# Kernel optimization log

Measured on AMD Instinct MI355X. Metric: run time of the kernel, lower is better.

The kernel has to match this reference:

```python
import jax, jax.numpy as jnp
import numpy as np

D_MODEL = 1024
NUM_HEADS = 16


def setup_inputs() -> dict:
    key = jax.random.key(0)
    ks = jax.random.split(key, 5)
    B, N, D = 2, 2048, D_MODEL
    x = jax.random.normal(ks[0], (B, N, D), dtype=jnp.float32)
    Wq = jax.random.normal(ks[1], (D, D), dtype=jnp.float32) * 0.02
    Wk = jax.random.normal(ks[2], (D, D), dtype=jnp.float32) * 0.02
    Wv = jax.random.normal(ks[3], (D, D), dtype=jnp.float32) * 0.02
    Wo = jax.random.normal(ks[4], (D, D), dtype=jnp.float32) * 0.02
    return {"x": x, "Wq": Wq, "Wk": Wk, "Wv": Wv, "Wo": Wo}


def reference(x, Wq, Wk, Wv, Wo):
    # Executed path of QuantizedHyperbolicAttention.forward: TRITON_AVAILABLE is
    # False in the source, so the module always runs _pytorch_attention
    # (standard scaled-dot-product attention), mask=None.
    B, N, D = x.shape
    H = NUM_HEADS
    hd = D // H
    # nn.Linear(bias=False): y = x @ W.T
    q = (x @ Wq.T).reshape(B, N, H, hd).transpose(0, 2, 1, 3)  # [B,H,N,hd]
    k = (x @ Wk.T).reshape(B, N, H, hd).transpose(0, 2, 1, 3)
    v = (x @ Wv.T).reshape(B, N, H, hd).transpose(0, 2, 1, 3)
    scale = hd ** -0.5
    attn = jnp.einsum("bhnd,bhmd->bhnm", q, k) * scale  # [B,H,N,N]
    attn = jax.nn.softmax(attn, axis=-1)
    out = jnp.einsum("bhnm,bhmd->bhnd", attn, v)  # [B,H,N,hd]
    out = out.transpose(0, 2, 1, 3).reshape(B, N, D)
    return out @ Wo.T
```

## Files before the change

kernel.cpp:

```cpp
#include <hip/hip_runtime.h>

using u16 = unsigned short;
using u32 = unsigned int;

typedef __bf16 bf16x8 __attribute__((ext_vector_type(8)));
typedef float  f32x4  __attribute__((ext_vector_type(4)));
typedef float  f32x8  __attribute__((ext_vector_type(8)));
typedef float  f32x16 __attribute__((ext_vector_type(16)));
typedef u16    u16x8  __attribute__((ext_vector_type(8)));
typedef u32    u32x4  __attribute__((ext_vector_type(4)));

__device__ __forceinline__ u32 f2bf(float f) {
  u32 u = __builtin_bit_cast(u32, f);
  return (u + 0x7fffu + ((u >> 16) & 1u)) >> 16;
}

__device__ __forceinline__ void gload_lds16(const u16* g, u16* lds) {
  __builtin_amdgcn_global_load_lds(
      (const __attribute__((address_space(1))) void*)g,
      (__attribute__((address_space(3))) void*)lds, 16, 0, 0);
}

__device__ __forceinline__ u32 cvtpk(float lo, float hi) {
  u32 r;
  asm("v_cvt_pk_bf16_f32 %0, %1, %2" : "=v"(r) : "v"(lo), "v"(hi));
  return r;
}

__device__ __forceinline__ float xhalf_add(float v) {
  return v + __shfl_xor(v, 32);
}

__global__ __launch_bounds__(256) void cvt_all(
    const float* __restrict__ x,  const float* __restrict__ wq,
    const float* __restrict__ wk, const float* __restrict__ wv,
    const float* __restrict__ wo, u16* __restrict__ out) {
  size_t i = ((size_t)blockIdx.x * 256 + threadIdx.x) * 8;
  const float* src;
  if (i < 4194304) {
    src = x + i;
  } else {
    size_t j = i - 4194304;
    unsigned w = (unsigned)(j >> 20);
    size_t o = j & 1048575;
    src = (w == 0) ? (wq + o) : (w == 1) ? (wk + o) : (w == 2) ? (wv + o) : (wo + o);
  }
  f32x4 a = *(const f32x4*)src;
  f32x4 b = *(const f32x4*)(src + 4);
  u32x4 r;
  r[0] = f2bf(a[0]) | (f2bf(a[1]) << 16);
  r[1] = f2bf(a[2]) | (f2bf(a[3]) << 16);
  r[2] = f2bf(b[0]) | (f2bf(b[1]) << 16);
  r[3] = f2bf(b[2]) | (f2bf(b[3]) << 16);
  *(u32x4*)(out + i) = r;
}

template <bool F32OUT>
__device__ __forceinline__ void gemm_tile(const u16* __restrict__ A,
                                          const u16* __restrict__ Bm,
                                          void* __restrict__ Cv,
                                          int rowBase, int colBase, float scale) {
  __shared__ __align__(16) u16 As[128 * 64];
  __shared__ __align__(16) u16 Bs[128 * 64];

  const int t = threadIdx.x;
  const int lane = t & 63;
  const int wv = t >> 6;
  const int wr = (wv >> 1) * 64;
  const int wc = (wv & 1) * 64;
  const int l15 = lane & 15;
  const int lg = lane >> 4;

  f32x4 acc[4][4] = {};

  for (int kt = 0; kt < 1024; kt += 64) {
#pragma unroll
    for (int i = 0; i < 4; ++i) {
      int s = i * 256 + t;
      int row = s >> 3;
      int k2 = (s & 7) ^ (row & 7);
      const u16* ga = A  + (size_t)(rowBase + row) * 1024 + kt + k2 * 8;
      const u16* gb = Bm + (size_t)(colBase + row) * 1024 + kt + k2 * 8;
      gload_lds16(ga, &As[(i * 256 + wv * 64) * 8]);
      gload_lds16(gb, &Bs[(i * 256 + wv * 64) * 8]);
    }
    __syncthreads();
#pragma unroll
    for (int kk = 0; kk < 2; ++kk) {
      bf16x8 af[4], bfr[4];
#pragma unroll
      for (int m = 0; m < 4; ++m) {
        int row = wr + m * 16 + l15;
        af[m] = *(const bf16x8*)&As[row * 64 + (((kk * 4 + lg) ^ (row & 7)) * 8)];
      }
#pragma unroll
      for (int n = 0; n < 4; ++n) {
        int row = wc + n * 16 + l15;
        bfr[n] = *(const bf16x8*)&Bs[row * 64 + (((kk * 4 + lg) ^ (row & 7)) * 8)];
      }
      __builtin_amdgcn_s_setprio(1);
#pragma unroll
      for (int m = 0; m < 4; ++m)
#pragma unroll
        for (int n = 0; n < 4; ++n)
          acc[m][n] = __builtin_amdgcn_mfma_f32_16x16x32_bf16(af[m], bfr[n], acc[m][n], 0, 0, 0);
      __builtin_amdgcn_s_setprio(0);
    }
    __syncthreads();
  }

#pragma unroll
  for (int m = 0; m < 4; ++m) {
#pragma unroll
    for (int r = 0; r < 4; ++r) {
      int row = rowBase + wr + m * 16 + lg * 4 + r;
#pragma unroll
      for (int n = 0; n < 4; ++n) {
        int col = colBase + wc + n * 16 + l15;
        float v = acc[m][n][r] * scale;
        if (F32OUT)
          ((float*)Cv)[(size_t)row * 1024 + col] = v;
        else
          ((u16*)Cv)[(size_t)row * 1024 + col] = (u16)f2bf(v);
      }
    }
  }
}

__global__ __launch_bounds__(256) void gemm_qkv(
    const u16* __restrict__ xb,
    const u16* __restrict__ wq, const u16* __restrict__ wk, const u16* __restrict__ wv,
    u16* __restrict__ Qm, u16* __restrict__ Km, u16* __restrict__ Vm) {
  int bx = blockIdx.x;
  int mat = bx >> 8;
  int rem = bx & 255;
  int bm = rem & 31, bn = rem >> 5;
  const u16* B = (mat == 0) ? wq : (mat == 1) ? wk : wv;
  u16* C = (mat == 0) ? Qm : (mat == 1) ? Km : Vm;
  float scale = (mat == 0) ? 0.125f : 1.0f;
  gemm_tile<false>(xb, B, C, bm * 128, bn * 128, scale);
}

__global__ __launch_bounds__(256) void gemm_out(
    const u16* __restrict__ ao, const u16* __restrict__ wo, float* __restrict__ C) {
  int bm = blockIdx.x & 31, bn = blockIdx.x >> 5;
  gemm_tile<true>(ao, wo, C, bm * 128, bn * 128, 1.0f);
}

__global__ __launch_bounds__(512, 2) void attn_fwd(
    const u16* __restrict__ Q, const u16* __restrict__ K,
    const u16* __restrict__ V, u16* __restrict__ AO) {
  __shared__ __align__(16) u16 Ks[2][2][64 * 64];
  __shared__ __align__(16) u16 Vt3[2][3][64 * 64];

  const int t = threadIdx.x;
  const int lane = t & 63;
  const int wvi = t >> 6;
  const int wg = wvi & 3;
  const int grp = wvi >> 2;
  const int tg = t & 255;
  const int l31 = lane & 31;
  const int hi = lane >> 5;

  const int qb = blockIdx.x;
  const int pr = blockIdx.y;
  const size_t hb = (size_t)(pr >> 4) * 2048 * 1024 + (size_t)(pr & 15) * 64;
  const u16* Qh = Q + hb;
  const u16* Kh = K + hb;
  const u16* Vh = V + hb;
  u16* AOh = AO + hb;

  const int q0w = qb * 128 + wg * 32;
  const int kvb = grp * 1024;

  bf16x8 qf[4];
#pragma unroll
  for (int kk = 0; kk < 4; ++kk)
    qf[kk] = *(const bf16x8*)&Qh[(size_t)(q0w + l31) * 1024 + kk * 16 + hi * 8];

  f32x16 ot[2] = {};
  f32x16 sc[2];
  f32x8  Lacc = {};
  bf16x8 pa0[4], pa1[4];

  const int kxor = l31 & 7;
  const int kd0 = (l31 & 7) ^ (l31 >> 3);
  const int kv0 = (tg >> 3) * 2, d0 = (tg & 7) * 8;
  const int vg = (kv0 >> 4) * 2 + ((kv0 >> 2) & 1);
  const int vj = (kv0 & 3) + ((kv0 >> 3) & 1) * 4;

  auto VLOAD = [&](int tile, u16x8& a, u16x8& b) {
    a = *(const u16x8*)&Vh[(size_t)(kvb + tile * 64 + kv0) * 1024 + d0];
    b = *(const u16x8*)&Vh[(size_t)(kvb + tile * 64 + kv0 + 1) * 1024 + d0];
  };
  auto KSTAGE = [&](int tile, int buf) {
#pragma unroll
    for (int i = 0; i < 2; ++i) {
      int s = i * 256 + tg;
      int krow = s >> 3;
      int k2 = (s & 7) ^ (krow & 7);
      gload_lds16(&Kh[(size_t)(kvb + tile * 64 + krow) * 1024 + k2 * 8],
                  &Ks[grp][buf][(i * 256 + wg * 64) * 8]);
    }
  };
  auto VPACK = [&](u16x8 a, u16x8 b, u16* dst) {
#pragma unroll
    for (int e = 0; e < 8; ++e) {
      int d = d0 + e;
      int key = ((d & 7) ^ (d >> 3)) & 7;
      int idx = d * 64 + ((vg ^ key) * 8) + vj;
      *(u32*)&dst[idx] = (u32)a[e] | ((u32)b[e] << 16);
    }
  };
  auto QKT = [&](const u16* ks) {
    sc[0] = f32x16{};
    sc[1] = f32x16{};
#pragma unroll
    for (int kk = 0; kk < 4; ++kk) {
      bf16x8 kf0 = *(const bf16x8*)&ks[l31 * 64 + (((kk * 2 + hi) ^ kxor) * 8)];
      bf16x8 kf1 = *(const bf16x8*)&ks[(32 + l31) * 64 + (((kk * 2 + hi) ^ kxor) * 8)];
      __builtin_amdgcn_s_setprio(1);
      sc[0] = __builtin_amdgcn_mfma_f32_32x32x16_bf16(kf0, qf[kk], sc[0], 0, 0, 0);
      sc[1] = __builtin_amdgcn_mfma_f32_32x32x16_bf16(kf1, qf[kk], sc[1], 0, 0, 0);
      __builtin_amdgcn_s_setprio(0);
    }
  };
  auto PV = [&](const u16* vt, const bf16x8* pa) {
#pragma unroll
    for (int kk = 0; kk < 4; ++kk) {
      bf16x8 vf0 = *(const bf16x8*)&vt[l31 * 64 + (((kk * 2 + hi) ^ kd0) * 8)];
      bf16x8 vf1 = *(const bf16x8*)&vt[(32 + l31) * 64 + (((kk * 2 + hi) ^ (kd0 ^ 4)) * 8)];
      __builtin_amdgcn_s_setprio(1);
      ot[0] = __builtin_amdgcn_mfma_f32_32x32x16_bf16(vf0, pa[kk], ot[0], 0, 0, 0);
      ot[1] = __builtin_amdgcn_mfma_f32_32x32x16_bf16(vf1, pa[kk], ot[1], 0, 0, 0);
      __builtin_amdgcn_s_setprio(0);
    }
  };
  auto EXPPACK = [&](bf16x8* pa) {
#pragma unroll
    for (int fi = 0; fi < 2; ++fi)
#pragma unroll
      for (int r = 0; r < 16; ++r)
        sc[fi][r] = __expf(sc[fi][r]);
    {
      f32x8 lo0 = __builtin_shufflevector(sc[0], sc[0], 0,1,2,3,4,5,6,7);
      f32x8 hi0 = __builtin_shufflevector(sc[0], sc[0], 8,9,10,11,12,13,14,15);
      f32x8 lo1 = __builtin_shufflevector(sc[1], sc[1], 0,1,2,3,4,5,6,7);
      f32x8 hi1 = __builtin_shufflevector(sc[1], sc[1], 8,9,10,11,12,13,14,15);
      Lacc += (lo0 + hi0) + (lo1 + hi1);
    }
#pragma unroll
    for (int fi = 0; fi < 2; ++fi) {
      u32x4 w0 = {cvtpk(sc[fi][0],  sc[fi][1]),  cvtpk(sc[fi][2],  sc[fi][3]),
                  cvtpk(sc[fi][4],  sc[fi][5]),  cvtpk(sc[fi][6],  sc[fi][7])};
      u32x4 w1 = {cvtpk(sc[fi][8],  sc[fi][9]),  cvtpk(sc[fi][10], sc[fi][11]),
                  cvtpk(sc[fi][12], sc[fi][13]), cvtpk(sc[fi][14], sc[fi][15])};
      pa[2 * fi]     = __builtin_bit_cast(bf16x8, w0);
      pa[2 * fi + 1] = __builtin_bit_cast(bf16x8, w1);
    }
  };

  int vm1 = 2, v0 = 0, vp1 = 1;
  auto ROT = [&]() { int tmp = vm1; vm1 = v0; v0 = vp1; vp1 = tmp; };

  {
    u16x8 a, b;
    VLOAD(0, a, b);
    __builtin_amdgcn_sched_barrier(0);
    KSTAGE(0, 0);
    KSTAGE(1, 1);
    VPACK(a, b, &Vt3[grp][0][0]);
    asm volatile("s_waitcnt vmcnt(2)" ::: "memory");
    asm volatile("s_waitcnt lgkmcnt(0)" ::: "memory");
    __builtin_amdgcn_sched_barrier(0);
    __builtin_amdgcn_s_barrier();
    QKT(&Ks[grp][0][0]);
    asm volatile("s_waitcnt lgkmcnt(0)" ::: "memory");
    __builtin_amdgcn_sched_barrier(0);
    __builtin_amdgcn_s_barrier();
  }

  for (int tp = 0; tp < 7; ++tp) {
#pragma unroll
    for (int sub = 0; sub < 2; ++sub) {
      const int tt = 2 * tp + sub;
      u16x8 a, b;
      VLOAD(tt + 1, a, b);
      __builtin_amdgcn_sched_barrier(0);
      KSTAGE(tt + 2, sub);
      if (tt >= 1) PV(&Vt3[grp][vm1][0], sub ? pa0 : pa1);
      EXPPACK(sub ? pa1 : pa0);
      asm volatile("s_waitcnt vmcnt(4)" ::: "memory");
      QKT(&Ks[grp][sub ^ 1][0]);
      VPACK(a, b, &Vt3[grp][vp1][0]);
      asm volatile("s_waitcnt lgkmcnt(0)" ::: "memory");
      __builtin_amdgcn_sched_barrier(0);
      __builtin_amdgcn_s_barrier();
      ROT();
    }
  }

  {
    u16x8 a, b;
    VLOAD(15, a, b);
    __builtin_amdgcn_sched_barrier(0);
    PV(&Vt3[grp][vm1][0], pa1);
    EXPPACK(pa0);
    asm volatile("s_waitcnt vmcnt(2)" ::: "memory");
    QKT(&Ks[grp][1][0]);
    VPACK(a, b, &Vt3[grp][vp1][0]);
    asm volatile("s_waitcnt lgkmcnt(0)" ::: "memory");
    __builtin_amdgcn_sched_barrier(0);
    __builtin_amdgcn_s_barrier();
    ROT();
  }
  PV(&Vt3[grp][vm1][0], pa0);
  EXPPACK(pa1);
  ROT();
  PV(&Vt3[grp][vm1][0], pa1);

  float lp = (((Lacc[0] + Lacc[1]) + (Lacc[2] + Lacc[3])) +
              ((Lacc[4] + Lacc[5]) + (Lacc[6] + Lacc[7])));

  __syncthreads();
  float* Osh = (float*)&Ks[0][0][0];
  float* Lsh = (float*)&Vt3[0][0][0];
  const int pair = wg;
  const int obase = (((pair * 2 + hi) * 32) + l31) * 32;
  if (grp == 1) {
    *(f32x16*)&Osh[obase]      = ot[0];
    *(f32x16*)&Osh[obase + 16] = ot[1];
    Lsh[pair * 64 + lane] = lp;
  }
  __syncthreads();
  if (grp == 0) {
    ot[0] += *(const f32x16*)&Osh[obase];
    ot[1] += *(const f32x16*)&Osh[obase + 16];
    lp += Lsh[pair * 64 + lane];
    float L = xhalf_add(lp);
    float inv = 1.f / L;
    const size_t qrow = (size_t)(q0w + l31) * 1024;
#pragma unroll
    for (int dn = 0; dn < 2; ++dn)
#pragma unroll
      for (int j = 0; j < 8; ++j) {
        int r = 2 * j;
        int d = 2 * (j & 1) + 8 * (j >> 1) + 4 * hi + 32 * dn;
        u32 w = cvtpk(ot[dn][r] * inv, ot[dn][r + 1] * inv);
        *(u32*)&AOh[qrow + d] = w;
      }
  }
}

extern "C" void kernel_launch(void* const* d_in, const int* in_sizes, int n_in,
                              void* d_out, int out_size, void* d_ws, size_t ws_size,
                              hipStream_t stream) {
  const float* x  = (const float*)d_in[0];
  const float* wq = (const float*)d_in[1];
  const float* wk = (const float*)d_in[2];
  const float* wv = (const float*)d_in[3];
  const float* wo = (const float*)d_in[4];

  u16* ws = (u16*)d_ws;
  u16* xb  = ws;
  u16* wqb = ws + 4194304;
  u16* wkb = ws + 5242880;
  u16* wvb = ws + 6291456;
  u16* wob = ws + 7340032;
  u16* Qm  = ws + 8388608;
  u16* Km  = ws + 12582912;
  u16* Vm  = ws + 16777216;
  u16* AOm = ws + 20971520;

  cvt_all<<<4096, 256, 0, stream>>>(x, wq, wk, wv, wo, ws);
  gemm_qkv<<<768, 256, 0, stream>>>(xb, wqb, wkb, wvb, Qm, Km, Vm);
  attn_fwd<<<dim3(16, 32), 512, 0, stream>>>(Qm, Km, Vm, AOm);
  gemm_out<<<256, 256, 0, stream>>>(AOm, wob, (float*)d_out);
}
```

Baseline: 112.7 us.

## Use exp2 with folded log2e scale, smaller out-GEMM tiles, wider convert, hoisted setprio

Result: faster. 106.6 us (-5.4%).

```diff
diff --git a/kernel.cpp b/kernel.cpp
--- a/kernel.cpp
+++ b/kernel.cpp
@@ -10,6 +10,14 @@
 typedef u16    u16x8  __attribute__((ext_vector_type(8)));
 typedef u32    u32x4  __attribute__((ext_vector_type(4)));
 
+#if __has_builtin(__builtin_amdgcn_exp2f)
+#define QSCALE 0.1803368801f
+__device__ __forceinline__ float fexp(float x) { return __builtin_amdgcn_exp2f(x); }
+#else
+#define QSCALE 0.125f
+__device__ __forceinline__ float fexp(float x) { return __expf(x); }
+#endif
+
 __device__ __forceinline__ u32 f2bf(float f) {
   u32 u = __builtin_bit_cast(u32, f);
   return (u + 0x7fffu + ((u >> 16) & 1u)) >> 16;
@@ -35,7 +43,7 @@
     const float* __restrict__ x,  const float* __restrict__ wq,
     const float* __restrict__ wk, const float* __restrict__ wv,
     const float* __restrict__ wo, u16* __restrict__ out) {
-  size_t i = ((size_t)blockIdx.x * 256 + threadIdx.x) * 8;
+  size_t i = ((size_t)blockIdx.x * 256 + threadIdx.x) * 16;
   const float* src;
   if (i < 4194304) {
     src = x + i;
@@ -47,49 +55,62 @@
   }
   f32x4 a = *(const f32x4*)src;
   f32x4 b = *(const f32x4*)(src + 4);
-  u32x4 r;
-  r[0] = f2bf(a[0]) | (f2bf(a[1]) << 16);
-  r[1] = f2bf(a[2]) | (f2bf(a[3]) << 16);
-  r[2] = f2bf(b[0]) | (f2bf(b[1]) << 16);
-  r[3] = f2bf(b[2]) | (f2bf(b[3]) << 16);
-  *(u32x4*)(out + i) = r;
-}
-
-template <bool F32OUT>
+  f32x4 c = *(const f32x4*)(src + 8);
+  f32x4 d = *(const f32x4*)(src + 12);
+  u32x4 r0, r1;
+  r0[0] = f2bf(a[0]) | (f2bf(a[1]) << 16);
+  r0[1] = f2bf(a[2]) | (f2bf(a[3]) << 16);
+  r0[2] = f2bf(b[0]) | (f2bf(b[1]) << 16);
+  r0[3] = f2bf(b[2]) | (f2bf(b[3]) << 16);
+  r1[0] = f2bf(c[0]) | (f2bf(c[1]) << 16);
+  r1[1] = f2bf(c[2]) | (f2bf(c[3]) << 16);
+  r1[2] = f2bf(d[0]) | (f2bf(d[1]) << 16);
+  r1[3] = f2bf(d[2]) | (f2bf(d[3]) << 16);
+  *(u32x4*)(out + i) = r0;
+  *(u32x4*)(out + i + 8) = r1;
+}
+
+template <bool F32OUT, int BM>
 __device__ __forceinline__ void gemm_tile(const u16* __restrict__ A,
                                           const u16* __restrict__ Bm,
                                           void* __restrict__ Cv,
                                           int rowBase, int colBase, float scale) {
-  __shared__ __align__(16) u16 As[128 * 64];
+  __shared__ __align__(16) u16 As[BM * 64];
   __shared__ __align__(16) u16 Bs[128 * 64];
 
   const int t = threadIdx.x;
   const int lane = t & 63;
   const int wv = t >> 6;
-  const int wr = (wv >> 1) * 64;
+  const int wr = (wv >> 1) * (BM / 2);
   const int wc = (wv & 1) * 64;
   const int l15 = lane & 15;
   const int lg = lane >> 4;
 
-  f32x4 acc[4][4] = {};
+  f32x4 acc[BM / 32][4] = {};
 
   for (int kt = 0; kt < 1024; kt += 64) {
+#pragma unroll
+    for (int i = 0; i < BM / 32; ++i) {
+      int s = i * 256 + t;
+      int row = s >> 3;
+      int k2 = (s & 7) ^ (row & 7);
+      gload_lds16(A + (size_t)(rowBase + row) * 1024 + kt + k2 * 8,
+                  &As[(i * 256 + wv * 64) * 8]);
+    }
 #pragma unroll
     for (int i = 0; i < 4; ++i) {
       int s = i * 256 + t;
       int row = s >> 3;
       int k2 = (s & 7) ^ (row & 7);
-      const u16* ga = A  + (size_t)(rowBase + row) * 1024 + kt + k2 * 8;
-      const u16* gb = Bm + (size_t)(colBase + row) * 1024 + kt + k2 * 8;
-      gload_lds16(ga, &As[(i * 256 + wv * 64) * 8]);
-      gload_lds16(gb, &Bs[(i * 256 + wv * 64) * 8]);
+      gload_lds16(Bm + (size_t)(colBase + row) * 1024 + kt + k2 * 8,
+                  &Bs[(i * 256 + wv * 64) * 8]);
     }
     __syncthreads();
 #pragma unroll
     for (int kk = 0; kk < 2; ++kk) {
-      bf16x8 af[4], bfr[4];
-#pragma unroll
-      for (int m = 0; m < 4; ++m) {
+      bf16x8 af[BM / 32], bfr[4];
+#pragma unroll
+      for (int m = 0; m < BM / 32; ++m) {
         int row = wr + m * 16 + l15;
         af[m] = *(const bf16x8*)&As[row * 64 + (((kk * 4 + lg) ^ (row & 7)) * 8)];
       }
@@ -100,7 +121,7 @@
       }
       __builtin_amdgcn_s_setprio(1);
 #pragma unroll
-      for (int m = 0; m < 4; ++m)
+      for (int m = 0; m < BM / 32; ++m)
 #pragma unroll
         for (int n = 0; n < 4; ++n)
           acc[m][n] = __builtin_amdgcn_mfma_f32_16x16x32_bf16(af[m], bfr[n], acc[m][n], 0, 0, 0);
@@ -110,7 +131,7 @@
   }
 
 #pragma unroll
-  for (int m = 0; m < 4; ++m) {
+  for (int m = 0; m < BM / 32; ++m) {
 #pragma unroll
     for (int r = 0; r < 4; ++r) {
       int row = rowBase + wr + m * 16 + lg * 4 + r;
@@ -137,14 +158,14 @@
   int bm = rem & 31, bn = rem >> 5;
   const u16* B = (mat == 0) ? wq : (mat == 1) ? wk : wv;
   u16* C = (mat == 0) ? Qm : (mat == 1) ? Km : Vm;
-  float scale = (mat == 0) ? 0.125f : 1.0f;
-  gemm_tile<false>(xb, B, C, bm * 128, bn * 128, scale);
+  float scale = (mat == 0) ? QSCALE : 1.0f;
+  gemm_tile<false, 128>(xb, B, C, bm * 128, bn * 128, scale);
 }
 
 __global__ __launch_bounds__(256) void gemm_out(
     const u16* __restrict__ ao, const u16* __restrict__ wo, float* __restrict__ C) {
-  int bm = blockIdx.x & 31, bn = blockIdx.x >> 5;
-  gemm_tile<true>(ao, wo, C, bm * 128, bn * 128, 1.0f);
+  int bm = blockIdx.x & 63, bn = blockIdx.x >> 6;
+  gemm_tile<true, 64>(ao, wo, C, bm * 64, bn * 128, 1.0f);
 }
 
 __global__ __launch_bounds__(512, 2) void attn_fwd(
@@ -215,33 +236,33 @@
   auto QKT = [&](const u16* ks) {
     sc[0] = f32x16{};
     sc[1] = f32x16{};
+    __builtin_amdgcn_s_setprio(1);
 #pragma unroll
     for (int kk = 0; kk < 4; ++kk) {
       bf16x8 kf0 = *(const bf16x8*)&ks[l31 * 64 + (((kk * 2 + hi) ^ kxor) * 8)];
       bf16x8 kf1 = *(const bf16x8*)&ks[(32 + l31) * 64 + (((kk * 2 + hi) ^ kxor) * 8)];
-      __builtin_amdgcn_s_setprio(1);
       sc[0] = __builtin_amdgcn_mfma_f32_32x32x16_bf16(kf0, qf[kk], sc[0], 0, 0, 0);
       sc[1] = __builtin_amdgcn_mfma_f32_32x32x16_bf16(kf1, qf[kk], sc[1], 0, 0, 0);
-      __builtin_amdgcn_s_setprio(0);
-    }
+    }
+    __builtin_amdgcn_s_setprio(0);
   };
   auto PV = [&](const u16* vt, const bf16x8* pa) {
+    __builtin_amdgcn_s_setprio(1);
 #pragma unroll
     for (int kk = 0; kk < 4; ++kk) {
       bf16x8 vf0 = *(const bf16x8*)&vt[l31 * 64 + (((kk * 2 + hi) ^ kd0) * 8)];
       bf16x8 vf1 = *(const bf16x8*)&vt[(32 + l31) * 64 + (((kk * 2 + hi) ^ (kd0 ^ 4)) * 8)];
-      __builtin_amdgcn_s_setprio(1);
       ot[0] = __builtin_amdgcn_mfma_f32_32x32x16_bf16(vf0, pa[kk], ot[0], 0, 0, 0);
       ot[1] = __builtin_amdgcn_mfma_f32_32x32x16_bf16(vf1, pa[kk], ot[1], 0, 0, 0);
-      __builtin_amdgcn_s_setprio(0);
-    }
+    }
+    __builtin_amdgcn_s_setprio(0);
   };
   auto EXPPACK = [&](bf16x8* pa) {
 #pragma unroll
     for (int fi = 0; fi < 2; ++fi)
 #pragma unroll
       for (int r = 0; r < 16; ++r)
-        sc[fi][r] = __expf(sc[fi][r]);
+        sc[fi][r] = fexp(sc[fi][r]);
     {
       f32x8 lo0 = __builtin_shufflevector(sc[0], sc[0], 0,1,2,3,4,5,6,7);
       f32x8 hi0 = __builtin_shufflevector(sc[0], sc[0], 8,9,10,11,12,13,14,15);
@@ -372,8 +393,8 @@
   u16* Vm  = ws + 16777216;
   u16* AOm = ws + 20971520;
 
-  cvt_all<<<4096, 256, 0, stream>>>(x, wq, wk, wv, wo, ws);
+  cvt_all<<<2048, 256, 0, stream>>>(x, wq, wk, wv, wo, ws);
   gemm_qkv<<<768, 256, 0, stream>>>(xb, wqb, wkb, wvb, Qm, Km, Vm);
   attn_fwd<<<dim3(16, 32), 512, 0, stream>>>(Qm, Km, Vm, AOm);
-  gemm_out<<<256, 256, 0, stream>>>(AOm, wob, (float*)d_out);
-}
+  gemm_out<<<512, 256, 0, stream>>>(AOm, wob, (float*)d_out);
+}
```
